# Kernel tuning notes

Measured on AMD Instinct MI355X. Metric: run time of the kernel, lower is better.

Reference implementation:

```python
import jax, jax.numpy as jnp
import numpy as np

B, T, K, D, V = 32, 200, 50, 100, 500000


def setup_inputs() -> dict:
    key = jax.random.key(0)
    k_ids, k_emb, k_wht, k_bht, k_wrel, k_brel = jax.random.split(key, 6)
    ids = jax.random.randint(k_ids, (B, T, K, 3), 0, V, dtype=jnp.int64)
    emb = jax.random.normal(k_emb, (V, D), dtype=jnp.float32) * 0.02
    # torch Linear weights are [out_features, in_features]
    W_ht = jax.random.normal(k_wht, (D, 2 * D), dtype=jnp.float32) * 0.05
    b_ht = jax.random.normal(k_bht, (D,), dtype=jnp.float32) * 0.05
    W_rel = jax.random.normal(k_wrel, (D, D), dtype=jnp.float32) * 0.05
    b_rel = jax.random.normal(k_brel, (D,), dtype=jnp.float32) * 0.05
    return {
        "batch_size": B,
        "one_two_triples_id": ids,
        "one_two_triple_num": T,
        "emb": emb,
        "W_ht": W_ht,
        "b_ht": b_ht,
        "W_rel": W_rel,
        "b_rel": b_rel,
    }


def reference(batch_size, one_two_triples_id, one_two_triple_num, emb, W_ht, b_ht, W_rel, b_rel):
    d = emb.shape[1]
    # gather: [B, T, K, 3, d] -> [B, T, K, 3d]
    tri = emb[one_two_triples_id].reshape(batch_size, one_two_triple_num, -1, 3 * d)
    head, relation, tail = jnp.split(tri, 3, axis=3)          # each [B,T,K,d]
    head_tail = jnp.concatenate([head, tail], axis=3)          # [B,T,K,2d]
    ht_t = jnp.tanh(jnp.einsum('btkf,df->btkd', head_tail, W_ht) + b_ht)
    rel_t = jnp.einsum('btke,de->btkd', relation, W_rel) + b_rel
    e_weight = jnp.sum(rel_t * ht_t, axis=3)                   # [B,T,K]
    alpha = jax.nn.softmax(e_weight, axis=2)                   # softmax over triples K
    one_two_embed = jnp.sum(alpha[..., None] * head_tail, axis=2)  # [B,T,2d]
    return one_two_embed
```

## Files before the change

### kernel.cpp

```cpp
#include <hip/hip_runtime.h>
#include <hip/hip_bf16.h>

#define KK 50
#define DD 100
#define TWO_D 200
#define DPAD 112
#define KHT 224
#define KRL 128

#define XHT_PITCH 232
#define XRL_PITCH 136

#define NCHUNK (KK * 3 * 25)

#define WS_FLAGS 0
#define WS_WHT 256
#define WS_WRL (WS_WHT + DPAD*KHT*2)
#define WS_BHT (WS_WRL + DPAD*KRL*2)
#define WS_BRL (WS_BHT + 256)

typedef __attribute__((ext_vector_type(8))) short   s8v;
typedef __attribute__((ext_vector_type(8))) __bf16  b8v;
typedef __attribute__((ext_vector_type(4))) __bf16  b4v;
typedef __attribute__((ext_vector_type(4))) float   f32x4;

template <typename T>
__device__ __forceinline__ auto mfma_try(T a, T b, f32x4 c, int)
    -> decltype(__builtin_amdgcn_mfma_f32_16x16x32_bf16(a, b, c, 0, 0, 0)) {
    return __builtin_amdgcn_mfma_f32_16x16x32_bf16(a, b, c, 0, 0, 0);
}
template <typename T, typename U = b8v>
__device__ __forceinline__ f32x4 mfma_try(T a, T b, f32x4 c, long) {
    U ab = __builtin_bit_cast(U, a);
    U bb = __builtin_bit_cast(U, b);
    return __builtin_amdgcn_mfma_f32_16x16x32_bf16(ab, bb, c, 0, 0, 0);
}
__device__ __forceinline__ f32x4 mfma16x16x32_bf16(s8v a, s8v b, f32x4 c) {
    return mfma_try(a, b, c, 0);
}

__device__ __forceinline__ float bf2f(__hip_bfloat16 h) { return __bfloat162float(h); }

__device__ __forceinline__ float tanh_fast(float x) {
    float e = __expf(2.f * x);
    return 1.f - 2.f * __builtin_amdgcn_rcpf(e + 1.f);
}

__global__ void detect_dtypes(const unsigned int* __restrict__ emb_raw,
                              const unsigned int* __restrict__ ids_raw,
                              int* __restrict__ flags) {
    const int lane = threadIdx.x;
    int f32 = 0;
    #pragma unroll
    for (int rep = 0; rep < 4; rep++) {
        unsigned int w = emb_raw[lane + rep * 64];
        unsigned int e0 = (w >> 7)  & 0xFF;
        unsigned int e1 = (w >> 23) & 0xFF;
        if (e0 >= 0x87 || e1 >= 0x87) f32 = 1;
    }
    unsigned long long mf = __ballot(f32 != 0);
    unsigned long long mz = __ballot(ids_raw[2 * lane + 1] == 0u);
    if (lane == 0) {
        flags[0] = mf ? 1 : 0;
        flags[1] = (__popcll(mz) >= 32) ? 1 : 0;
    }
}

__global__ void prep_weights(const void* __restrict__ Wht, const void* __restrict__ bht,
                             const void* __restrict__ Wrl, const void* __restrict__ brl,
                             void* __restrict__ ws) {
    const int* flags = (const int*)ws;
    const bool f32 = flags[0] != 0;
    __hip_bfloat16* whtp = (__hip_bfloat16*)((char*)ws + WS_WHT);
    __hip_bfloat16* wrlp = (__hip_bfloat16*)((char*)ws + WS_WRL);
    __hip_bfloat16* bhtp = (__hip_bfloat16*)((char*)ws + WS_BHT);
    __hip_bfloat16* brlp = (__hip_bfloat16*)((char*)ws + WS_BRL);

    const int gid = blockIdx.x * blockDim.x + threadIdx.x;
    const int gs  = gridDim.x * blockDim.x;

    for (int i = gid; i < DPAD * KHT; i += gs) {
        int d = i / KHT, f = i - d * KHT;
        float v = 0.f;
        if (d < DD && f < TWO_D)
            v = f32 ? ((const float*)Wht)[d * TWO_D + f]
                    : bf2f(((const __hip_bfloat16*)Wht)[d * TWO_D + f]);
        whtp[i] = __float2bfloat16(v);
    }
    for (int i = gid; i < DPAD * KRL; i += gs) {
        int d = i / KRL, f = i - d * KRL;
        float v = 0.f;
        if (d < DD && f < DD)
            v = f32 ? ((const float*)Wrl)[d * DD + f]
                    : bf2f(((const __hip_bfloat16*)Wrl)[d * DD + f]);
        wrlp[i] = __float2bfloat16(v);
    }
    for (int i = gid; i < DPAD; i += gs) {
        float vh = 0.f, vr = 0.f;
        if (i < DD) {
            vh = f32 ? ((const float*)bht)[i] : bf2f(((const __hip_bfloat16*)bht)[i]);
            vr = f32 ? ((const float*)brl)[i] : bf2f(((const __hip_bfloat16*)brl)[i]);
        }
        bhtp[i] = __float2bfloat16(vh);
        brlp[i] = __float2bfloat16(vr);
    }
}

#define XHT_BYTES (KK * XHT_PITCH * 2)
#define XRL_BYTES (KK * XRL_PITCH * 2)

__device__ __forceinline__ int gather_dst_off(int c) {
    int seg = c / 25;
    int off = (c - seg * 25) * 4;
    int r = seg / 3, wh = seg - r * 3;
    if (wh == 1) return XHT_BYTES + (r * XRL_PITCH + off) * 2;
    return (r * XHT_PITCH + (wh ? DD : 0) + off) * 2;
}

template <int CNT>
__device__ __forceinline__ void gather_f32(const float* __restrict__ embf,
                                           const int* __restrict__ sIds,
                                           char* sX, int tid, int base) {
    float4 v[CNT];
    int doff[CNT];
    #pragma unroll
    for (int i = 0; i < CNT; ++i) {
        int c = tid + (base + i) * 256;
        bool ok = (c < NCHUNK);
        int cc = ok ? c : 0;
        int seg = cc / 25;
        int off = (cc - seg * 25) * 4;
        size_t id = (size_t)sIds[seg];
        v[i] = *(const float4*)(embf + id * DD + off);
        doff[i] = ok ? gather_dst_off(cc) : -1;
    }
    #pragma unroll
    for (int i = 0; i < CNT; ++i) {
        if (doff[i] >= 0) {
            b4v pk = { (__bf16)v[i].x, (__bf16)v[i].y, (__bf16)v[i].z, (__bf16)v[i].w };
            *(b4v*)(sX + doff[i]) = pk;
        }
    }
}

template <int CNT>
__device__ __forceinline__ void gather_bf16(const __hip_bfloat16* __restrict__ embh,
                                            const int* __restrict__ sIds,
                                            char* sX, int tid, int base) {
    uint2 v[CNT];
    int doff[CNT];
    #pragma unroll
    for (int i = 0; i < CNT; ++i) {
        int c = tid + (base + i) * 256;
        bool ok = (c < NCHUNK);
        int cc = ok ? c : 0;
        int seg = cc / 25;
        int off = (cc - seg * 25) * 4;
        size_t id = (size_t)sIds[seg];
        v[i] = *(const uint2*)(embh + id * DD + off);
        doff[i] = ok ? gather_dst_off(cc) : -1;
    }
    #pragma unroll
    for (int i = 0; i < CNT; ++i) {
        if (doff[i] >= 0) *(uint2*)(sX + doff[i]) = v[i];
    }
}

__global__ __launch_bounds__(256, 4) void fused_outer_encoder(
    const int* __restrict__ ids,
    const void* __restrict__ emb_raw,
    const void* __restrict__ ws,
    float* __restrict__ out)
{
    __shared__ char sX[XHT_BYTES + XRL_BYTES];
    __shared__ int   sIds[KK * 3];
    __shared__ float sE[64];
    __shared__ float sAl[KK];
    __hip_bfloat16* sXht = (__hip_bfloat16*)sX;
    __hip_bfloat16* sXrl = (__hip_bfloat16*)(sX + XHT_BYTES);

    const int* flags = (const int*)ws;
    const __hip_bfloat16* whtp = (const __hip_bfloat16*)((const char*)ws + WS_WHT);
    const __hip_bfloat16* wrlp = (const __hip_bfloat16*)((const char*)ws + WS_WRL);
    const __hip_bfloat16* bhtp = (const __hip_bfloat16*)((const char*)ws + WS_BHT);
    const __hip_bfloat16* brlp = (const __hip_bfloat16*)((const char*)ws + WS_BRL);

    const int tid = threadIdx.x;
    const int bt  = blockIdx.x;
    const bool f32      = flags[0] != 0;
    const int idsStride = flags[1] ? 2 : 1;

    int myid = 0;
    if (tid < KK * 3) myid = ids[(bt * (KK * 3) + tid) * idsStride];

    for (int i = tid; i < KK * 16; i += 256) {
        int r = i >> 4, cw = i & 15;
        ((unsigned int*)(sXht + r * XHT_PITCH + 200))[cw] = 0u;
    }
    for (int i = tid; i < KK * 18; i += 256) {
        int r = i / 18, cw = i - r * 18;
        ((unsigned int*)(sXrl + r * XRL_PITCH + 100))[cw] = 0u;
    }
    if (tid < KK * 3) sIds[tid] = myid;
    __syncthreads();

    if (f32) {
        const float* embf = (const float*)emb_raw;
        gather_f32<8>(embf, sIds, sX, tid, 0);
        gather_f32<7>(embf, sIds, sX, tid, 8);
    } else {
        const __hip_bfloat16* embh = (const __hip_bfloat16*)emb_raw;
        gather_bf16<8>(embh, sIds, sX, tid, 0);
        gather_bf16<7>(embh, sIds, sX, tid, 8);
    }
    __syncthreads();

    const int lane = tid & 63;
    const int w    = tid >> 6;
    const int n    = lane & 15;
    const int q    = lane >> 4;
    const int arow = w * 16 + n;
    const int arc  = (arow < KK) ? arow : 0;

    f32x4 accH[7];
    #pragma unroll
    for (int t = 0; t < 7; t++) {
        #pragma unroll
        for (int j = 0; j < 4; j++) accH[t][j] = 0.f;
    }
    #pragma unroll
    for (int ks = 0; ks < 7; ks++) {
        s8v a = *(const s8v*)(sXht + arc * XHT_PITCH + ks * 32 + q * 8);
        #pragma unroll
        for (int nt = 0; nt < 7; nt++) {
            s8v b = *(const s8v*)(whtp + (nt * 16 + n) * KHT + ks * 32 + q * 8);
            accH[nt] = mfma16x16x32_bf16(a, b, accH[nt]);
        }
    }

    float htv[7][4];
    #pragma unroll
    for (int nt = 0; nt < 7; nt++) {
        const float bias = bf2f(bhtp[nt * 16 + n]);
        #pragma unroll
        for (int j = 0; j < 4; j++) htv[nt][j] = tanh_fast(accH[nt][j] + bias);
    }

    f32x4 accR[7];
    #pragma unroll
    for (int t = 0; t < 7; t++) {
        #pragma unroll
        for (int j = 0; j < 4; j++) accR[t][j] = 0.f;
    }
    #pragma unroll
    for (int ks = 0; ks < 4; ks++) {
        s8v a = *(const s8v*)(sXrl + arc * XRL_PITCH + ks * 32 + q * 8);
        #pragma unroll
        for (int nt = 0; nt < 7; nt++) {
            s8v b = *(const s8v*)(wrlp + (nt * 16 + n) * KRL + ks * 32 + q * 8);
            accR[nt] = mfma16x16x32_bf16(a, b, accR[nt]);
        }
    }

    float dj[4];
    #pragma unroll
    for (int j = 0; j < 4; j++) dj[j] = 0.f;
    #pragma unroll
    for (int nt = 0; nt < 7; nt++) {
        const float bias = bf2f(brlp[nt * 16 + n]);
        #pragma unroll
        for (int j = 0; j < 4; j++) dj[j] += (accR[nt][j] + bias) * htv[nt][j];
    }
    #pragma unroll
    for (int mask = 1; mask < 16; mask <<= 1) {
        #pragma unroll
        for (int j = 0; j < 4; j++) dj[j] += __shfl_xor(dj[j], mask, 64);
    }
    if (n == 0) {
        #pragma unroll
        for (int j = 0; j < 4; j++) {
            const int kt = w * 16 + q * 4 + j;
            if (kt < KK) sE[kt] = dj[j];
        }
    }
    __syncthreads();

    if (tid < 64) {
        float v = (tid < KK) ? sE[tid] : -3.0e38f;
        float mx = v;
        #pragma unroll
        for (int mask = 1; mask < 64; mask <<= 1) mx = fmaxf(mx, __shfl_xor(mx, mask, 64));
        float p = (tid < KK) ? __expf(v - mx) : 0.f;
        float s = p;
        #pragma unroll
        for (int mask = 1; mask < 64; mask <<= 1) s += __shfl_xor(s, mask, 64);
        if (tid < KK) sAl[tid] = p / s;
    }
    __syncthreads();

    if (tid < TWO_D) {
        const int half  = tid / DD;
        const int dmod  = tid - half * DD;
        const int whoff = half ? 2 : 0;
        float acc = 0.f;
        if (f32) {
            const float* embf = (const float*)emb_raw;
            #pragma unroll 10
            for (int k = 0; k < KK; k++) {
                size_t id = (size_t)sIds[k * 3 + whoff];
                acc += sAl[k] * embf[id * DD + dmod];
            }
        } else {
            const __hip_bfloat16* embh = (const __hip_bfloat16*)emb_raw;
            #pragma unroll 10
            for (int k = 0; k < KK; k++) {
                size_t id = (size_t)sIds[k * 3 + whoff];
                acc += sAl[k] * bf2f(embh[id * DD + dmod]);
            }
        }
        out[(size_t)bt * TWO_D + tid] = acc;
    }
}

extern "C" void kernel_launch(void* const* d_in, const int* in_sizes, int n_in,
                              void* d_out, int out_size, void* d_ws, size_t ws_size,
                              hipStream_t stream) {
    const int*  ids = (const int*)d_in[1];
    const void* emb = d_in[3];
    const void* Wht = d_in[4];
    const void* bht = d_in[5];
    const void* Wrl = d_in[6];
    const void* brl = d_in[7];
    float* out = (float*)d_out;

    const int nbt = in_sizes[1] / (KK * 3);

    hipLaunchKernelGGL(detect_dtypes, dim3(1), dim3(64), 0, stream,
                       (const unsigned int*)emb, (const unsigned int*)ids, (int*)d_ws);
    hipLaunchKernelGGL(prep_weights, dim3(64), dim3(256), 0, stream,
                       Wht, bht, Wrl, brl, d_ws);
    hipLaunchKernelGGL(fused_outer_encoder, dim3(nbt), dim3(256), 0, stream,
                       ids, emb, (const void*)d_ws, out);
}
```

Before: 449.0 us.

## Unify smem row layout and split GEMM into two passes to cut registers

The gathered embeddings now go into one shared buffer with a uniform 104-element pitch per head/relation/tail row, replacing the separate head-tail and relation buffers with their own pitches. The W_ht packing is remapped to match this layout, and the A fragment addressing is adjusted so the tail half starts two rows later. The output tiles are computed in two passes (4 then 3) that fuse tanh and the dot product, so fewer accumulators are live at once, and launch bounds rise from 4 to 5 blocks per SM. The intent is lower shared memory and register use for higher occupancy, plus simpler gather addressing. The cost is reloading the A fragments in the second pass, and the odd 104-element pitch may cause LDS bank conflicts.

```diff
diff --git a/kernel.cpp b/kernel.cpp
--- a/kernel.cpp
+++ b/kernel.cpp
@@ -8,10 +8,11 @@
 #define KHT 224
 #define KRL 128
 
-#define XHT_PITCH 232
-#define XRL_PITCH 136
-
-#define NCHUNK (KK * 3 * 25)
+#define NROWS 150
+#define ROWP 104
+#define SX_ELEMS ((NROWS + 1) * ROWP)
+
+#define NCHUNK (NROWS * 25)
 
 #define WS_FLAGS 0
 #define WS_WHT 256
@@ -81,10 +82,13 @@
 
     for (int i = gid; i < DPAD * KHT; i += gs) {
         int d = i / KHT, f = i - d * KHT;
+        int src = -1;
+        if (f < 112) { if (f < DD) src = f; }
+        else { int t = f - 112; if (t < DD) src = DD + t; }
         float v = 0.f;
-        if (d < DD && f < TWO_D)
-            v = f32 ? ((const float*)Wht)[d * TWO_D + f]
-                    : bf2f(((const __hip_bfloat16*)Wht)[d * TWO_D + f]);
+        if (d < DD && src >= 0)
+            v = f32 ? ((const float*)Wht)[d * TWO_D + src]
+                    : bf2f(((const __hip_bfloat16*)Wht)[d * TWO_D + src]);
         whtp[i] = __float2bfloat16(v);
     }
     for (int i = gid; i < DPAD * KRL; i += gs) {
@@ -106,21 +110,10 @@
     }
 }
 
-#define XHT_BYTES (KK * XHT_PITCH * 2)
-#define XRL_BYTES (KK * XRL_PITCH * 2)
-
-__device__ __forceinline__ int gather_dst_off(int c) {
-    int seg = c / 25;
-    int off = (c - seg * 25) * 4;
-    int r = seg / 3, wh = seg - r * 3;
-    if (wh == 1) return XHT_BYTES + (r * XRL_PITCH + off) * 2;
-    return (r * XHT_PITCH + (wh ? DD : 0) + off) * 2;
-}
-
 template <int CNT>
 __device__ __forceinline__ void gather_f32(const float* __restrict__ embf,
                                            const int* __restrict__ sIds,
-                                           char* sX, int tid, int base) {
+                                           __hip_bfloat16* sX, int tid, int base) {
     float4 v[CNT];
     int doff[CNT];
     #pragma unroll
@@ -132,7 +125,7 @@
         int off = (cc - seg * 25) * 4;
         size_t id = (size_t)sIds[seg];
         v[i] = *(const float4*)(embf + id * DD + off);
-        doff[i] = ok ? gather_dst_off(cc) : -1;
+        doff[i] = ok ? (seg * ROWP + off) : -1;
     }
     #pragma unroll
     for (int i = 0; i < CNT; ++i) {
@@ -146,7 +139,7 @@
 template <int CNT>
 __device__ __forceinline__ void gather_bf16(const __hip_bfloat16* __restrict__ embh,
                                             const int* __restrict__ sIds,
-                                            char* sX, int tid, int base) {
+                                            __hip_bfloat16* sX, int tid, int base) {
     uint2 v[CNT];
     int doff[CNT];
     #pragma unroll
@@ -158,7 +151,7 @@
         int off = (cc - seg * 25) * 4;
         size_t id = (size_t)sIds[seg];
         v[i] = *(const uint2*)(embh + id * DD + off);
-        doff[i] = ok ? gather_dst_off(cc) : -1;
+        doff[i] = ok ? (seg * ROWP + off) : -1;
     }
     #pragma unroll
     for (int i = 0; i < CNT; ++i) {
@@ -166,18 +159,69 @@
     }
 }
 
-__global__ __launch_bounds__(256, 4) void fused_outer_encoder(
+template <int NTP>
+__device__ __forceinline__ void gemm_pass(
+    const __hip_bfloat16* __restrict__ sX,
+    const __hip_bfloat16* __restrict__ whtp, const __hip_bfloat16* __restrict__ wrlp,
+    const __hip_bfloat16* __restrict__ bhtp, const __hip_bfloat16* __restrict__ brlp,
+    int hbase, int n, int q, int ntBase, float dj[4]) {
+
+    f32x4 accH[NTP];
+    #pragma unroll
+    for (int t = 0; t < NTP; t++) {
+        #pragma unroll
+        for (int j = 0; j < 4; j++) accH[t][j] = 0.f;
+    }
+    #pragma unroll
+    for (int ks = 0; ks < 7; ks++) {
+        const int  c    = ks * 4 + q;
+        const bool ish  = (c < 14);
+        const int  eoff = ish ? (hbase + c * 8) : (hbase + 2 * ROWP + (c - 14) * 8);
+        s8v a = *(const s8v*)(sX + eoff);
+        #pragma unroll
+        for (int nt = 0; nt < NTP; nt++) {
+            s8v b = *(const s8v*)(whtp + ((ntBase + nt) * 16 + n) * KHT + ks * 32 + q * 8);
+            accH[nt] = mfma16x16x32_bf16(a, b, accH[nt]);
+        }
+    }
+
+    f32x4 accR[NTP];
+    #pragma unroll
+    for (int t = 0; t < NTP; t++) {
+        #pragma unroll
+        for (int j = 0; j < 4; j++) accR[t][j] = 0.f;
+    }
+    #pragma unroll
+    for (int ks = 0; ks < 4; ks++) {
+        const int c = ks * 4 + q;
+        s8v a = *(const s8v*)(sX + hbase + ROWP + c * 8);
+        #pragma unroll
+        for (int nt = 0; nt < NTP; nt++) {
+            s8v b = *(const s8v*)(wrlp + ((ntBase + nt) * 16 + n) * KRL + ks * 32 + q * 8);
+            accR[nt] = mfma16x16x32_bf16(a, b, accR[nt]);
+        }
+    }
+
+    #pragma unroll
+    for (int nt = 0; nt < NTP; nt++) {
+        const float bh = bf2f(bhtp[(ntBase + nt) * 16 + n]);
+        const float br = bf2f(brlp[(ntBase + nt) * 16 + n]);
+        #pragma unroll
+        for (int j = 0; j < 4; j++)
+            dj[j] += (accR[nt][j] + br) * tanh_fast(accH[nt][j] + bh);
+    }
+}
+
+__global__ __launch_bounds__(256, 5) void fused_outer_encoder(
     const int* __restrict__ ids,
     const void* __restrict__ emb_raw,
     const void* __restrict__ ws,
     float* __restrict__ out)
 {
-    __shared__ char sX[XHT_BYTES + XRL_BYTES];
+    __shared__ __hip_bfloat16 sX[SX_ELEMS];
     __shared__ int   sIds[KK * 3];
     __shared__ float sE[64];
     __shared__ float sAl[KK];
-    __hip_bfloat16* sXht = (__hip_bfloat16*)sX;
-    __hip_bfloat16* sXrl = (__hip_bfloat16*)(sX + XHT_BYTES);
 
     const int* flags = (const int*)ws;
     const __hip_bfloat16* whtp = (const __hip_bfloat16*)((const char*)ws + WS_WHT);
@@ -191,17 +235,13 @@
     const int idsStride = flags[1] ? 2 : 1;
 
     int myid = 0;
-    if (tid < KK * 3) myid = ids[(bt * (KK * 3) + tid) * idsStride];
-
-    for (int i = tid; i < KK * 16; i += 256) {
-        int r = i >> 4, cw = i & 15;
-        ((unsigned int*)(sXht + r * XHT_PITCH + 200))[cw] = 0u;
-    }
-    for (int i = tid; i < KK * 18; i += 256) {
-        int r = i / 18, cw = i - r * 18;
-        ((unsigned int*)(sXrl + r * XRL_PITCH + 100))[cw] = 0u;
-    }
-    if (tid < KK * 3) sIds[tid] = myid;
+    if (tid < NROWS) myid = ids[(bt * NROWS + tid) * idsStride];
+
+    for (int i = tid; i < 176; i += 256) {
+        if (i < 151) *(uint2*)((char*)sX + i * (ROWP * 2) + 200) = make_uint2(0u, 0u);
+        else         *(uint2*)((char*)sX + NROWS * (ROWP * 2) + (i - 151) * 8) = make_uint2(0u, 0u);
+    }
+    if (tid < NROWS) sIds[tid] = myid;
     __syncthreads();
 
     if (f32) {
@@ -221,56 +261,12 @@
     const int q    = lane >> 4;
     const int arow = w * 16 + n;
     const int arc  = (arow < KK) ? arow : 0;
-
-    f32x4 accH[7];
-    #pragma unroll
-    for (int t = 0; t < 7; t++) {
-        #pragma unroll
-        for (int j = 0; j < 4; j++) accH[t][j] = 0.f;
-    }
-    #pragma unroll
-    for (int ks = 0; ks < 7; ks++) {
-        s8v a = *(const s8v*)(sXht + arc * XHT_PITCH + ks * 32 + q * 8);
-        #pragma unroll
-        for (int nt = 0; nt < 7; nt++) {
-            s8v b = *(const s8v*)(whtp + (nt * 16 + n) * KHT + ks * 32 + q * 8);
-            accH[nt] = mfma16x16x32_bf16(a, b, accH[nt]);
-        }
-    }
-
-    float htv[7][4];
-    #pragma unroll
-    for (int nt = 0; nt < 7; nt++) {
-        const float bias = bf2f(bhtp[nt * 16 + n]);
-        #pragma unroll
-        for (int j = 0; j < 4; j++) htv[nt][j] = tanh_fast(accH[nt][j] + bias);
-    }
-
-    f32x4 accR[7];
-    #pragma unroll
-    for (int t = 0; t < 7; t++) {
-        #pragma unroll
-        for (int j = 0; j < 4; j++) accR[t][j] = 0.f;
-    }
-    #pragma unroll
-    for (int ks = 0; ks < 4; ks++) {
-        s8v a = *(const s8v*)(sXrl + arc * XRL_PITCH + ks * 32 + q * 8);
-        #pragma unroll
-        for (int nt = 0; nt < 7; nt++) {
-            s8v b = *(const s8v*)(wrlp + (nt * 16 + n) * KRL + ks * 32 + q * 8);
-            accR[nt] = mfma16x16x32_bf16(a, b, accR[nt]);
-        }
-    }
-
-    float dj[4];
-    #pragma unroll
-    for (int j = 0; j < 4; j++) dj[j] = 0.f;
-    #pragma unroll
-    for (int nt = 0; nt < 7; nt++) {
-        const float bias = bf2f(brlp[nt * 16 + n]);
-        #pragma unroll
-        for (int j = 0; j < 4; j++) dj[j] += (accR[nt][j] + bias) * htv[nt][j];
-    }
+    const int hbase = 3 * arc * ROWP;
+
+    float dj[4] = {0.f, 0.f, 0.f, 0.f};
+    gemm_pass<4>(sX, whtp, wrlp, bhtp, brlp, hbase, n, q, 0, dj);
+    gemm_pass<3>(sX, whtp, wrlp, bhtp, brlp, hbase, n, q, 4, dj);
+
     #pragma unroll
     for (int mask = 1; mask < 16; mask <<= 1) {
         #pragma unroll
```

Result: slower. 512.4 us (+14.1%).
